# Kernel tuning notes

Hardware: AMD Instinct MI355X
Metric: run time of the kernel (lower is better)

The kernel has to match this reference:

```python
import jax, jax.numpy as jnp
import numpy as np

DROPOUT_P = 0.5
NUM_NODES = 50000


def _gcn_layer(x, W, b, src, dst, ew, num_nodes):
    # support = x @ W ; out = A_hat @ support + b, with A_hat given as edge list
    h = x @ W                               # [N, out_dim]
    msg = h[src] * ew[:, None]              # [E, out_dim]
    agg = jax.ops.segment_sum(msg, dst, num_segments=num_nodes)  # [N, out_dim]
    return agg + b


def setup_inputs() -> dict:
    key = jax.random.key(0)
    ks = jax.random.split(key, 8)
    N, E, F_in, H, C = NUM_NODES, 800000, 512, 128, 64
    x = jax.random.normal(ks[0], (N, F_in), dtype=jnp.float32)
    edge_weight = jax.random.uniform(ks[1], (E,), dtype=jnp.float32)
    W1 = jax.random.normal(ks[2], (F_in, H), dtype=jnp.float32) * (1.0 / np.sqrt(F_in))
    b1 = jax.random.normal(ks[3], (H,), dtype=jnp.float32) * 0.01
    W2 = jax.random.normal(ks[4], (H, C), dtype=jnp.float32) * (1.0 / np.sqrt(H))
    b2 = jax.random.normal(ks[5], (C,), dtype=jnp.float32) * 0.01
    drop_mask = jax.random.uniform(ks[6], (N, H), dtype=jnp.float32)
    edge_index = jax.random.randint(ks[7], (2, E), 0, N, dtype=jnp.int32)
    return {"x": x, "edge_weight": edge_weight, "W1": W1, "b1": b1,
            "W2": W2, "b2": b2, "drop_mask": drop_mask, "edge_index": edge_index}


def reference(x, edge_weight, W1, b1, W2, b2, drop_mask, edge_index):
    src, dst = edge_index[0], edge_index[1]
    h = _gcn_layer(x, W1, b1, src, dst, edge_weight, NUM_NODES)
    h = jax.nn.relu(h)
    # deterministic inverted dropout using precomputed uniform mask
    keep = (drop_mask >= DROPOUT_P).astype(h.dtype)
    h = h * keep / (1.0 - DROPOUT_P)
    h = _gcn_layer(h, W2, b2, src, dst, edge_weight, NUM_NODES)
    return jax.nn.log_softmax(h, axis=1)
```

## Files before the change

kernel.cpp:

```cpp
#include <hip/hip_runtime.h>
#include <cstdint>
#include <cstddef>

constexpr int FIN = 512;
constexpr int HD  = 128;
constexpr int CD  = 64;
constexpr int NREP = 8;

typedef __attribute__((ext_vector_type(8))) short short8;
typedef __attribute__((ext_vector_type(4))) float f32x4;

__device__ inline unsigned short f2bf(float f) {
  unsigned int u = __float_as_uint(f);
  u += 0x7fffu + ((u >> 16) & 1u);
  return (unsigned short)(u >> 16);
}
__device__ inline float bf_lo(unsigned int v) { return __uint_as_float(v << 16); }
__device__ inline float bf_hi(unsigned int v) { return __uint_as_float(v & 0xffff0000u); }
__device__ inline float bf1(unsigned short v) { return __uint_as_float((unsigned int)v << 16); }


__global__ __launch_bounds__(256) void prep(const float* __restrict__ W1,
                                            const float* __restrict__ W2,
                                            unsigned short* __restrict__ w1t,
                                            unsigned short* __restrict__ w2t,
                                            int* __restrict__ cnt, int n8) {
  int idx = blockIdx.x * 256 + threadIdx.x;
  if (idx < FIN * HD) {
    int k = idx >> 7, c = idx & 127;
    w1t[(size_t)c * FIN + k] = f2bf(W1[idx]);
  } else if (idx < FIN * HD + HD * CD) {
    int j = idx - FIN * HD;
    int k = j >> 6, c = j & 63;
    w2t[(size_t)c * HD + k] = f2bf(W2[j]);
  }
  if (idx < n8) cnt[idx] = 0;
}


__global__ __launch_bounds__(256) void scan_a(const int* __restrict__ cnt,
                                              int* __restrict__ bs, int n) {
  __shared__ int sh[256];
  int t = threadIdx.x;
  int base = blockIdx.x * 2048;
  int s = 0;
#pragma unroll
  for (int j = 0; j < 8; ++j) {
    int idx = base + j * 256 + t;
    if (idx < n) {
#pragma unroll
      for (int r = 0; r < NREP; ++r) s += cnt[(size_t)r * n + idx];
    }
  }
  sh[t] = s;
  __syncthreads();
  for (int o = 128; o > 0; o >>= 1) {
    if (t < o) sh[t] += sh[t + o];
    __syncthreads();
  }
  if (t == 0) bs[blockIdx.x] = sh[0];
}

__global__ __launch_bounds__(256) void scan_c(const int* __restrict__ cnt,
                                              const int* __restrict__ bs,
                                              int* __restrict__ off,
                                              int* __restrict__ cur,
                                              int* __restrict__ deg, int n) {
  __shared__ int sh[256];
  __shared__ int sbase;
  const int t   = threadIdx.x;
  const int bid = blockIdx.x;
  if (t < 64) {
    int v = (t < bid) ? bs[t] : 0;
#pragma unroll
    for (int o = 32; o > 0; o >>= 1) v += __shfl_xor(v, o, 64);
    if (t == 0) sbase = v;
  }
  const int base = bid * 2048 + t * 8;
  int v[8];
  int local = 0;
#pragma unroll
  for (int j = 0; j < 8; ++j) {
    int s = 0;
    if (base + j < n) {
#pragma unroll
      for (int r = 0; r < NREP; ++r) s += cnt[(size_t)r * n + base + j];
    }
    v[j] = s;
    local += s;
  }
  sh[t] = local;
  __syncthreads();
  for (int o = 1; o < 256; o <<= 1) {
    int u = (t >= o) ? sh[t - o] : 0;
    __syncthreads();
    sh[t] += u;
    __syncthreads();
  }
  int run = sbase + sh[t] - local;
#pragma unroll
  for (int j = 0; j < 8; ++j) {
    if (base + j < n) { off[base + j] = run; cur[base + j] = run; deg[base + j] = v[j]; }
    run += v[j];
  }
}


__global__ __launch_bounds__(256) void scatter_kernel(const int* __restrict__ src,
                                                      const int* __restrict__ dst,
                                                      const float* __restrict__ ew, int E,
                                                      int* __restrict__ cur,
                                                      int2* __restrict__ sew) {
  int i = blockIdx.x * 256 + threadIdx.x;
  if (i < E) {
    int d = dst[i];
    int p = atomicAdd(&cur[d], 1);
    sew[p] = make_int2(src[i], __float_as_int(ew[i]));
  }
}


__global__ __launch_bounds__(256) void gemm1_mfma(const float* __restrict__ x,
                                                  const unsigned short* __restrict__ w1t,
                                                  unsigned short* __restrict__ h1b, int M,
                                                  const int* __restrict__ dst, int E,
                                                  int* __restrict__ cnt, int Nn) {
  {
    int* rep = cnt + (size_t)(blockIdx.x & (NREP - 1)) * Nn;
    const int stride = gridDim.x * 256;
    for (int i = blockIdx.x * 256 + threadIdx.x; i < E; i += stride)
      atomicAdd(&rep[dst[i]], 1);
  }

  __shared__ unsigned short As[64][72];
  __shared__ unsigned short Bs[128][72];
  const int t    = threadIdx.x;
  const int wave = t >> 6;
  const int lane = t & 63;
  const int l15  = lane & 15;
  const int quad = lane >> 4;
  const int m0   = blockIdx.x * 64;

  const int ar = t >> 2;
  const int ak = (t & 3) * 16;
  const int br = t >> 1;
  const int bk = (t & 1) * 32;

  const bool aok = (m0 + ar) < M;
  const float* xrow = x + (size_t)(m0 + ar) * FIN + ak;
  const unsigned short* brow = w1t + (size_t)br * FIN + bk;

  f32x4 acc[8];
#pragma unroll
  for (int j = 0; j < 8; ++j) acc[j] = (f32x4)0.f;

  float4 pa0 = make_float4(0.f, 0.f, 0.f, 0.f), pa1 = pa0, pa2 = pa0, pa3 = pa0;
  if (aok) {
    pa0 = *(const float4*)(xrow + 0);
    pa1 = *(const float4*)(xrow + 4);
    pa2 = *(const float4*)(xrow + 8);
    pa3 = *(const float4*)(xrow + 12);
  }
  uint4 pb0 = *(const uint4*)(brow + 0);
  uint4 pb1 = *(const uint4*)(brow + 8);
  uint4 pb2 = *(const uint4*)(brow + 16);
  uint4 pb3 = *(const uint4*)(brow + 24);

  for (int k0 = 0; k0 < FIN; k0 += 64) {
    __syncthreads();
    unsigned short tmp[16];
    tmp[0]  = f2bf(pa0.x); tmp[1]  = f2bf(pa0.y); tmp[2]  = f2bf(pa0.z); tmp[3]  = f2bf(pa0.w);
    tmp[4]  = f2bf(pa1.x); tmp[5]  = f2bf(pa1.y); tmp[6]  = f2bf(pa1.z); tmp[7]  = f2bf(pa1.w);
    tmp[8]  = f2bf(pa2.x); tmp[9]  = f2bf(pa2.y); tmp[10] = f2bf(pa2.z); tmp[11] = f2bf(pa2.w);
    tmp[12] = f2bf(pa3.x); tmp[13] = f2bf(pa3.y); tmp[14] = f2bf(pa3.z); tmp[15] = f2bf(pa3.w);
    *(uint4*)&As[ar][ak]      = ((const uint4*)tmp)[0];
    *(uint4*)&As[ar][ak + 8]  = ((const uint4*)tmp)[1];
    *(uint4*)&Bs[br][bk]      = pb0;
    *(uint4*)&Bs[br][bk + 8]  = pb1;
    *(uint4*)&Bs[br][bk + 16] = pb2;
    *(uint4*)&Bs[br][bk + 24] = pb3;
    __syncthreads();

    const bool more = (k0 + 64) < FIN;
    float4 qa0 = make_float4(0.f, 0.f, 0.f, 0.f), qa1 = qa0, qa2 = qa0, qa3 = qa0;
    uint4 qb0 = make_uint4(0, 0, 0, 0), qb1 = qb0, qb2 = qb0, qb3 = qb0;
    if (more) {
      if (aok) {
        qa0 = *(const float4*)(xrow + k0 + 64);
        qa1 = *(const float4*)(xrow + k0 + 68);
        qa2 = *(const float4*)(xrow + k0 + 72);
        qa3 = *(const float4*)(xrow + k0 + 76);
      }
      qb0 = *(const uint4*)(brow + k0 + 64);
      qb1 = *(const uint4*)(brow + k0 + 72);
      qb2 = *(const uint4*)(brow + k0 + 80);
      qb3 = *(const uint4*)(brow + k0 + 88);
    }

#pragma unroll
    for (int ks = 0; ks < 64; ks += 32) {
      short8 af = *(const short8*)&As[wave * 16 + l15][ks + quad * 8];
#pragma unroll
      for (int nt = 0; nt < 8; ++nt) {
        short8 bf = *(const short8*)&Bs[nt * 16 + l15][ks + quad * 8];
        acc[nt] = __builtin_amdgcn_mfma_f32_16x16x32_bf16(af, bf, acc[nt], 0, 0, 0);
      }
    }
    pa0 = qa0; pa1 = qa1; pa2 = qa2; pa3 = qa3;
    pb0 = qb0; pb1 = qb1; pb2 = qb2; pb3 = qb3;
  }
  const int row0 = m0 + wave * 16 + quad * 4;
#pragma unroll
  for (int r = 0; r < 4; ++r) {
    int row = row0 + r;
    if (row < M) {
      unsigned short* orow = h1b + (size_t)row * HD + l15;
#pragma unroll
      for (int nt = 0; nt < 8; ++nt) orow[nt * 16] = f2bf(acc[nt][r]);
    }
  }
}


__global__ __launch_bounds__(256) void agg1_kernel(const unsigned int* __restrict__ h1b,
                                                   const float* __restrict__ b1,
                                                   const float* __restrict__ dm,
                                                   const int* __restrict__ off,
                                                   const int* __restrict__ cnt,
                                                   const int2* __restrict__ sew,
                                                   unsigned int* __restrict__ hbf, int N) {
  const int wave = threadIdx.x >> 6;
  const int lane = threadIdx.x & 63;
  const int node = blockIdx.x * 4 + wave;
  if (node >= N) return;
  const int start = off[node];
  const int deg   = cnt[node];
  const int2* ep  = sew + start;

  float a0 = 0.f, a1 = 0.f, c0 = 0.f, c1 = 0.f;
  float e0 = 0.f, e1 = 0.f, g0 = 0.f, g1 = 0.f;
  int e = 0;
  for (; e + 8 <= deg; e += 8) {
    int2 p0 = ep[e + 0], p1 = ep[e + 1], p2 = ep[e + 2], p3 = ep[e + 3];
    int2 p4 = ep[e + 4], p5 = ep[e + 5], p6 = ep[e + 6], p7 = ep[e + 7];
    unsigned int v0 = h1b[(size_t)p0.x * 64 + lane];
    unsigned int v1 = h1b[(size_t)p1.x * 64 + lane];
    unsigned int v2 = h1b[(size_t)p2.x * 64 + lane];
    unsigned int v3 = h1b[(size_t)p3.x * 64 + lane];
    unsigned int v4 = h1b[(size_t)p4.x * 64 + lane];
    unsigned int v5 = h1b[(size_t)p5.x * 64 + lane];
    unsigned int v6 = h1b[(size_t)p6.x * 64 + lane];
    unsigned int v7 = h1b[(size_t)p7.x * 64 + lane];
    float w0 = __int_as_float(p0.y), w1 = __int_as_float(p1.y);
    float w2 = __int_as_float(p2.y), w3 = __int_as_float(p3.y);
    float w4 = __int_as_float(p4.y), w5 = __int_as_float(p5.y);
    float w6 = __int_as_float(p6.y), w7 = __int_as_float(p7.y);
    a0 = fmaf(bf_lo(v0), w0, a0); a1 = fmaf(bf_hi(v0), w0, a1);
    c0 = fmaf(bf_lo(v1), w1, c0); c1 = fmaf(bf_hi(v1), w1, c1);
    e0 = fmaf(bf_lo(v2), w2, e0); e1 = fmaf(bf_hi(v2), w2, e1);
    g0 = fmaf(bf_lo(v3), w3, g0); g1 = fmaf(bf_hi(v3), w3, g1);
    a0 = fmaf(bf_lo(v4), w4, a0); a1 = fmaf(bf_hi(v4), w4, a1);
    c0 = fmaf(bf_lo(v5), w5, c0); c1 = fmaf(bf_hi(v5), w5, c1);
    e0 = fmaf(bf_lo(v6), w6, e0); e1 = fmaf(bf_hi(v6), w6, e1);
    g0 = fmaf(bf_lo(v7), w7, g0); g1 = fmaf(bf_hi(v7), w7, g1);
  }
  for (; e + 4 <= deg; e += 4) {
    int2 p0 = ep[e + 0], p1 = ep[e + 1], p2 = ep[e + 2], p3 = ep[e + 3];
    unsigned int v0 = h1b[(size_t)p0.x * 64 + lane];
    unsigned int v1 = h1b[(size_t)p1.x * 64 + lane];
    unsigned int v2 = h1b[(size_t)p2.x * 64 + lane];
    unsigned int v3 = h1b[(size_t)p3.x * 64 + lane];
    float w0 = __int_as_float(p0.y), w1 = __int_as_float(p1.y);
    float w2 = __int_as_float(p2.y), w3 = __int_as_float(p3.y);
    a0 = fmaf(bf_lo(v0), w0, a0); a1 = fmaf(bf_hi(v0), w0, a1);
    c0 = fmaf(bf_lo(v1), w1, c0); c1 = fmaf(bf_hi(v1), w1, c1);
    e0 = fmaf(bf_lo(v2), w2, e0); e1 = fmaf(bf_hi(v2), w2, e1);
    g0 = fmaf(bf_lo(v3), w3, g0); g1 = fmaf(bf_hi(v3), w3, g1);
  }
  for (; e < deg; ++e) {
    int2 p = ep[e];
    unsigned int v = h1b[(size_t)p.x * 64 + lane];
    float w = __int_as_float(p.y);
    a0 = fmaf(bf_lo(v), w, a0); a1 = fmaf(bf_hi(v), w, a1);
  }
  a0 += c0 + e0 + g0; a1 += c1 + e1 + g1;

  const int f0 = lane * 2;
  float2 bb = *(const float2*)(b1 + f0);
  float2 dd = *(const float2*)(dm + (size_t)node * HD + f0);
  float r0 = fmaxf(a0 + bb.x, 0.f) * ((dd.x >= 0.5f) ? 2.0f : 0.0f);
  float r1 = fmaxf(a1 + bb.y, 0.f) * ((dd.y >= 0.5f) ? 2.0f : 0.0f);
  hbf[(size_t)node * 64 + lane] = (unsigned int)f2bf(r0) | ((unsigned int)f2bf(r1) << 16);
}


__global__ __launch_bounds__(256) void gemm2_mfma(const unsigned short* __restrict__ hbf,
                                                  const unsigned short* __restrict__ w2t,
                                                  unsigned short* __restrict__ h2b, int M) {
  __shared__ unsigned short As[128][40];
  __shared__ unsigned short Bs[64][40];
  const int t    = threadIdx.x;
  const int wave = t >> 6;
  const int lane = t & 63;
  const int l15  = lane & 15;
  const int quad = lane >> 4;
  const int m0   = blockIdx.x * 128;

  const int sr = t >> 1;
  const int sk = (t & 1) * 16;
  const int rb = t >> 2;
  const int kb = (t & 3) * 8;

  const bool aok = (m0 + sr) < M;
  const unsigned short* arow = hbf + (size_t)(m0 + sr) * HD + sk;
  const unsigned short* brow = w2t + (size_t)rb * HD + kb;

  f32x4 acc[2][4];
#pragma unroll
  for (int i = 0; i < 2; ++i)
#pragma unroll
    for (int j = 0; j < 4; ++j) acc[i][j] = (f32x4)0.f;

  for (int k0 = 0; k0 < HD; k0 += 32) {
    uint4 av0 = make_uint4(0, 0, 0, 0), av1 = av0;
    if (aok) {
      av0 = *(const uint4*)(arow + k0);
      av1 = *(const uint4*)(arow + k0 + 8);
    }
    uint4 bv = *(const uint4*)(brow + k0);
    __syncthreads();
    *(uint4*)&As[sr][sk]     = av0;
    *(uint4*)&As[sr][sk + 8] = av1;
    *(uint4*)&Bs[rb][kb]     = bv;
    __syncthreads();
    short8 af0 = *(const short8*)&As[wave * 32 + l15][quad * 8];
    short8 af1 = *(const short8*)&As[wave * 32 + 16 + l15][quad * 8];
#pragma unroll
    for (int nt = 0; nt < 4; ++nt) {
      short8 bf = *(const short8*)&Bs[nt * 16 + l15][quad * 8];
      acc[0][nt] = __builtin_amdgcn_mfma_f32_16x16x32_bf16(af0, bf, acc[0][nt], 0, 0, 0);
      acc[1][nt] = __builtin_amdgcn_mfma_f32_16x16x32_bf16(af1, bf, acc[1][nt], 0, 0, 0);
    }
  }
#pragma unroll
  for (int mt = 0; mt < 2; ++mt) {
    const int row0 = m0 + wave * 32 + mt * 16 + quad * 4;
#pragma unroll
    for (int r = 0; r < 4; ++r) {
      int row = row0 + r;
      if (row < M) {
        unsigned short* orow = h2b + (size_t)row * CD + l15;
#pragma unroll
        for (int nt = 0; nt < 4; ++nt) orow[nt * 16] = f2bf(acc[mt][nt][r]);
      }
    }
  }
}


__global__ __launch_bounds__(256) void agg2_kernel(const unsigned short* __restrict__ h2b,
                                                   const float* __restrict__ b2,
                                                   const int* __restrict__ off,
                                                   const int* __restrict__ cnt,
                                                   const int2* __restrict__ sew,
                                                   float* __restrict__ out, int N) {
  const int wave = threadIdx.x >> 6;
  const int c    = threadIdx.x & 63;
  const int node = blockIdx.x * 4 + wave;
  if (node >= N) return;
  const int start = off[node];
  const int deg   = cnt[node];
  const int2* ep  = sew + start;

  float acc = b2[c], a1 = 0.f, a2 = 0.f, a3 = 0.f;
  int e = 0;
  for (; e + 8 <= deg; e += 8) {
    int2 p0 = ep[e + 0], p1 = ep[e + 1], p2 = ep[e + 2], p3 = ep[e + 3];
    int2 p4 = ep[e + 4], p5 = ep[e + 5], p6 = ep[e + 6], p7 = ep[e + 7];
    float v0 = bf1(h2b[(size_t)p0.x * CD + c]);
    float v1 = bf1(h2b[(size_t)p1.x * CD + c]);
    float v2 = bf1(h2b[(size_t)p2.x * CD + c]);
    float v3 = bf1(h2b[(size_t)p3.x * CD + c]);
    float v4 = bf1(h2b[(size_t)p4.x * CD + c]);
    float v5 = bf1(h2b[(size_t)p5.x * CD + c]);
    float v6 = bf1(h2b[(size_t)p6.x * CD + c]);
    float v7 = bf1(h2b[(size_t)p7.x * CD + c]);
    acc = fmaf(v0, __int_as_float(p0.y), acc);
    a1  = fmaf(v1, __int_as_float(p1.y), a1);
    a2  = fmaf(v2, __int_as_float(p2.y), a2);
    a3  = fmaf(v3, __int_as_float(p3.y), a3);
    acc = fmaf(v4, __int_as_float(p4.y), acc);
    a1  = fmaf(v5, __int_as_float(p5.y), a1);
    a2  = fmaf(v6, __int_as_float(p6.y), a2);
    a3  = fmaf(v7, __int_as_float(p7.y), a3);
  }
  for (; e + 4 <= deg; e += 4) {
    int2 p0 = ep[e + 0], p1 = ep[e + 1], p2 = ep[e + 2], p3 = ep[e + 3];
    float v0 = bf1(h2b[(size_t)p0.x * CD + c]);
    float v1 = bf1(h2b[(size_t)p1.x * CD + c]);
    float v2 = bf1(h2b[(size_t)p2.x * CD + c]);
    float v3 = bf1(h2b[(size_t)p3.x * CD + c]);
    acc = fmaf(v0, __int_as_float(p0.y), acc);
    a1  = fmaf(v1, __int_as_float(p1.y), a1);
    a2  = fmaf(v2, __int_as_float(p2.y), a2);
    a3  = fmaf(v3, __int_as_float(p3.y), a3);
  }
  for (; e < deg; ++e) {
    int2 p = ep[e];
    acc = fmaf(bf1(h2b[(size_t)p.x * CD + c]), __int_as_float(p.y), acc);
  }
  acc += a1 + a2 + a3;

  float m = acc;
#pragma unroll
  for (int o = 32; o > 0; o >>= 1) m = fmaxf(m, __shfl_xor(m, o, 64));
  float ex = __expf(acc - m);
  float ssum = ex;
#pragma unroll
  for (int o = 32; o > 0; o >>= 1) ssum += __shfl_xor(ssum, o, 64);
  out[(size_t)node * CD + c] = (acc - m) - __logf(ssum);
}


extern "C" void kernel_launch(void* const* d_in, const int* in_sizes, int n_in,
                              void* d_out, int out_size, void* d_ws, size_t ws_size,
                              hipStream_t stream) {
  const float* x  = (const float*)d_in[0];
  const float* ew = (const float*)d_in[1];
  const float* W1 = (const float*)d_in[2];
  const float* b1 = (const float*)d_in[3];
  const float* W2 = (const float*)d_in[4];
  const float* b2 = (const float*)d_in[5];
  const float* dm = (const float*)d_in[6];
  const int*   ei = (const int*)d_in[7];
  float* out = (float*)d_out;

  const int E = in_sizes[1];
  const int N = in_sizes[6] / HD;
  const int* srcp = ei;
  const int* dstp = ei + E;
  const int nb = (N + 2047) / 2048;

  uint8_t* w = (uint8_t*)d_ws;
  size_t o = 0;
  auto alloc = [&](size_t bytes) -> void* {
    void* p = w + o;
    o = (o + bytes + 255) & ~(size_t)255;
    return p;
  };
  int*   off    = (int*)alloc((size_t)N * 4);
  int*   cnt    = (int*)alloc((size_t)NREP * N * 4);
  int*   cur    = (int*)alloc((size_t)N * 4);
  int*   deg    = (int*)alloc((size_t)N * 4);
  int2*  sew    = (int2*)alloc((size_t)E * 8);
  unsigned short* h1b = (unsigned short*)alloc((size_t)N * HD * 2);
  unsigned int*   hbf = (unsigned int*)alloc((size_t)N * HD * 2);
  unsigned short* h2b = (unsigned short*)alloc((size_t)N * CD * 2);
  unsigned short* w1t = (unsigned short*)alloc((size_t)FIN * HD * 2);
  unsigned short* w2t = (unsigned short*)alloc((size_t)HD * CD * 2);
  int*   bsum   = (int*)alloc((size_t)nb * 4);

  const int wcvt = FIN * HD + HD * CD;
  const int prep_threads = (wcvt > NREP * N) ? wcvt : NREP * N;
  prep<<<(prep_threads + 255) / 256, 256, 0, stream>>>(W1, W2, w1t, w2t, cnt, NREP * N);
  gemm1_mfma<<<(N + 63) / 64, 256, 0, stream>>>(x, w1t, h1b, N, dstp, E, cnt, N);
  scan_a<<<nb, 256, 0, stream>>>(cnt, bsum, N);
  scan_c<<<nb, 256, 0, stream>>>(cnt, bsum, off, cur, deg, N);
  scatter_kernel<<<(E + 255) / 256, 256, 0, stream>>>(srcp, dstp, ew, E, cur, sew);
  agg1_kernel<<<(N + 3) / 4, 256, 0, stream>>>((const unsigned int*)h1b, b1, dm, off, deg, sew, hbf, N);
  gemm2_mfma<<<(N + 127) / 128, 256, 0, stream>>>((const unsigned short*)hbf, w2t, h2b, N);
  agg2_kernel<<<(N + 3) / 4, 256, 0, stream>>>(h2b, b2, off, deg, sew, out, N);
}
```

Baseline: 361.2 us.

## Split degree histogram out of gemm1 and stage gemm1 output through LDS

Moves the destination-degree atomic histogram from the head of the gemm1 kernel into a separate kernel, so the GEMM no longer stalls on scattered atomics before starting its math. The gemm1 epilogue now writes bf16 results to a shared-memory tile and stores full rows with 16-byte vector writes instead of scattered 2-byte stores. The A-tile bf16 conversion is also repacked into 32-bit pairs. The cost is an extra kernel launch, the loss of overlap between the histogram and the GEMM, and 16 KB more LDS per block, which may reduce occupancy.

```diff
diff --git a/kernel.cpp b/kernel.cpp
--- a/kernel.cpp
+++ b/kernel.cpp
@@ -14,6 +14,9 @@
   unsigned int u = __float_as_uint(f);
   u += 0x7fffu + ((u >> 16) & 1u);
   return (unsigned short)(u >> 16);
+}
+__device__ inline unsigned int pk2(float lo, float hi) {
+  return (unsigned int)f2bf(lo) | ((unsigned int)f2bf(hi) << 16);
 }
 __device__ inline float bf_lo(unsigned int v) { return __uint_as_float(v << 16); }
 __device__ inline float bf_hi(unsigned int v) { return __uint_as_float(v & 0xffff0000u); }
@@ -38,6 +41,14 @@
 }
 
 
+__global__ __launch_bounds__(256) void hist_kernel(const int* __restrict__ dst, int E,
+                                                   int* __restrict__ cnt, int Nn) {
+  int* rep = cnt + (size_t)(blockIdx.x & (NREP - 1)) * Nn;
+  int i = blockIdx.x * 256 + threadIdx.x;
+  if (i < E) atomicAdd(&rep[dst[i]], 1);
+}
+
+
 __global__ __launch_bounds__(256) void scan_a(const int* __restrict__ cnt,
                                               int* __restrict__ bs, int n) {
   __shared__ int sh[256];
@@ -122,18 +133,10 @@
 
 __global__ __launch_bounds__(256) void gemm1_mfma(const float* __restrict__ x,
                                                   const unsigned short* __restrict__ w1t,
-                                                  unsigned short* __restrict__ h1b, int M,
-                                                  const int* __restrict__ dst, int E,
-                                                  int* __restrict__ cnt, int Nn) {
-  {
-    int* rep = cnt + (size_t)(blockIdx.x & (NREP - 1)) * Nn;
-    const int stride = gridDim.x * 256;
-    for (int i = blockIdx.x * 256 + threadIdx.x; i < E; i += stride)
-      atomicAdd(&rep[dst[i]], 1);
-  }
-
+                                                  unsigned short* __restrict__ h1b, int M) {
   __shared__ unsigned short As[64][72];
   __shared__ unsigned short Bs[128][72];
+  __shared__ unsigned short Out[64][128];
   const int t    = threadIdx.x;
   const int wave = t >> 6;
   const int lane = t & 63;
@@ -168,13 +171,13 @@
 
   for (int k0 = 0; k0 < FIN; k0 += 64) {
     __syncthreads();
-    unsigned short tmp[16];
-    tmp[0]  = f2bf(pa0.x); tmp[1]  = f2bf(pa0.y); tmp[2]  = f2bf(pa0.z); tmp[3]  = f2bf(pa0.w);
-    tmp[4]  = f2bf(pa1.x); tmp[5]  = f2bf(pa1.y); tmp[6]  = f2bf(pa1.z); tmp[7]  = f2bf(pa1.w);
-    tmp[8]  = f2bf(pa2.x); tmp[9]  = f2bf(pa2.y); tmp[10] = f2bf(pa2.z); tmp[11] = f2bf(pa2.w);
-    tmp[12] = f2bf(pa3.x); tmp[13] = f2bf(pa3.y); tmp[14] = f2bf(pa3.z); tmp[15] = f2bf(pa3.w);
-    *(uint4*)&As[ar][ak]      = ((const uint4*)tmp)[0];
-    *(uint4*)&As[ar][ak + 8]  = ((const uint4*)tmp)[1];
+    uint4 av0, av1;
+    av0.x = pk2(pa0.x, pa0.y); av0.y = pk2(pa0.z, pa0.w);
+    av0.z = pk2(pa1.x, pa1.y); av0.w = pk2(pa1.z, pa1.w);
+    av1.x = pk2(pa2.x, pa2.y); av1.y = pk2(pa2.z, pa2.w);
+    av1.z = pk2(pa3.x, pa3.y); av1.w = pk2(pa3.z, pa3.w);
+    *(uint4*)&As[ar][ak]      = av0;
+    *(uint4*)&As[ar][ak + 8]  = av1;
     *(uint4*)&Bs[br][bk]      = pb0;
     *(uint4*)&Bs[br][bk + 8]  = pb1;
     *(uint4*)&Bs[br][bk + 16] = pb2;
@@ -209,15 +212,27 @@
     pa0 = qa0; pa1 = qa1; pa2 = qa2; pa3 = qa3;
     pb0 = qb0; pb1 = qb1; pb2 = qb2; pb3 = qb3;
   }
-  const int row0 = m0 + wave * 16 + quad * 4;
-#pragma unroll
-  for (int r = 0; r < 4; ++r) {
-    int row = row0 + r;
-    if (row < M) {
-      unsigned short* orow = h1b + (size_t)row * HD + l15;
-#pragma unroll
-      for (int nt = 0; nt < 8; ++nt) orow[nt * 16] = f2bf(acc[nt][r]);
-    }
+
+  const int orow = wave * 16 + quad * 4;
+#pragma unroll
+  for (int nt = 0; nt < 8; ++nt)
+#pragma unroll
+    for (int r = 0; r < 4; ++r)
+      Out[orow + r][nt * 16 + l15] = f2bf(acc[nt][r]);
+  __syncthreads();
+  const int sr_o = t >> 2;
+  const int sc_o = (t & 3) * 32;
+  const int grow = m0 + sr_o;
+  if (grow < M) {
+    uint4 v0 = *(const uint4*)&Out[sr_o][sc_o];
+    uint4 v1 = *(const uint4*)&Out[sr_o][sc_o + 8];
+    uint4 v2 = *(const uint4*)&Out[sr_o][sc_o + 16];
+    uint4 v3 = *(const uint4*)&Out[sr_o][sc_o + 24];
+    unsigned short* op = h1b + (size_t)grow * HD + sc_o;
+    *(uint4*)(op)      = v0;
+    *(uint4*)(op + 8)  = v1;
+    *(uint4*)(op + 16) = v2;
+    *(uint4*)(op + 24) = v3;
   }
 }
 
@@ -463,7 +478,8 @@
   const int wcvt = FIN * HD + HD * CD;
   const int prep_threads = (wcvt > NREP * N) ? wcvt : NREP * N;
   prep<<<(prep_threads + 255) / 256, 256, 0, stream>>>(W1, W2, w1t, w2t, cnt, NREP * N);
-  gemm1_mfma<<<(N + 63) / 64, 256, 0, stream>>>(x, w1t, h1b, N, dstp, E, cnt, N);
+  hist_kernel<<<(E + 255) / 256, 256, 0, stream>>>(dstp, E, cnt, N);
+  gemm1_mfma<<<(N + 63) / 64, 256, 0, stream>>>(x, w1t, h1b, N);
   scan_a<<<nb, 256, 0, stream>>>(cnt, bsum, N);
   scan_c<<<nb, 256, 0, stream>>>(cnt, bsum, off, cur, deg, N);
   scatter_kernel<<<(E + 255) / 256, 256, 0, stream>>>(srcp, dstp, ew, E, cur, sew);
```

Measured after the change: 365.7 us. About the same (+1.3%).
